# Optimization experiments

Measured on AMD Instinct MI355X. Metric: run time of the kernel, lower is better.

The kernel has to match this reference:

```python
import jax, jax.numpy as jnp
import numpy as np

D = 128        # d_model (LayerNorm(128) hardcoded)
N_HEADS = 4
DIM_K = D // N_HEADS           # 32
HD = DIM_K // N_HEADS          # 8 = per-group dim after reshape(-1, B, S, HD)
NORM_FACT = 1.0 / np.sqrt(DIM_K)
HIDDEN = 512
LN_EPS = 1e-5
NEG_INF = -1e30


def layer_norm(x, g, b):
    mu = jnp.mean(x, axis=-1, keepdims=True)
    var = jnp.mean((x - mu) ** 2, axis=-1, keepdims=True)
    return (x - mu) * jax.lax.rsqrt(var + LN_EPS) * g + b


def lower_median(x):
    # torch.median(dim=-1) returns the LOWER of the two middle values for even n
    n = x.shape[-1]
    return jnp.sort(x, axis=-1)[..., (n - 1) // 2][..., None]


def cross_cov_attention(x, y, Wq, bq, Wk, bk, Wv, bv, Wo, bo):
    # x: query-side input [B,S,D]; y: key/value-side input [B,S,D]
    B, S, _ = x.shape
    Q = (x @ Wq + bq).reshape(-1, B, S, HD)   # [16,B,S,8] (raw row-major reshape, as in torch)
    K = (y @ Wk + bk).reshape(-1, B, S, HD)
    V = (y @ Wv + bv).reshape(-1, B, S, HD)
    Qn = Q / jnp.maximum(jnp.linalg.norm(Q, axis=-1, keepdims=True), 1e-12)
    Kn = K / jnp.maximum(jnp.linalg.norm(K, axis=-1, keepdims=True), 1e-12)
    # channel-wise cross-covariance: Q^T K over tokens -> [16,B,8,8]
    scores = jnp.einsum('gbsd,gbse->gbde', Qn, Kn) * NORM_FACT
    # median-threshold mask: keep entries strictly above the (lower) median of each row
    med = lower_median(scores)
    scores = jnp.where(scores - med > 0, scores, NEG_INF)
    probs = jax.nn.softmax(scores, axis=-1)
    # probs @ V^T -> [16,B,8,S]
    ao = jnp.einsum('gbde,gbse->gbds', probs, V)
    # torch: .transpose(-2,-1).transpose(1,2).view(B,S,-1)  == axes (g,b,d,s)->(g,s,b,d)->reshape
    ao = ao.transpose(0, 3, 1, 2).reshape(B, S, -1)  # [B,S,128]
    return ao @ Wo + bo


def setup_inputs() -> dict:
    key = jax.random.key(0)
    ks = jax.random.split(key, 16)
    B, S = 32, 4096
    s = 1.0 / np.sqrt(D)
    inp = {
        'q': jax.random.normal(ks[0], (B, S, D), jnp.float32),
        'v': jax.random.normal(ks[1], (B, S, D), jnp.float32),
        'Wq': jax.random.normal(ks[2], (D, D), jnp.float32) * s,
        'bq': jnp.zeros((D,), jnp.float32),
        'Wk': jax.random.normal(ks[3], (D, D), jnp.float32) * s,
        'bk': jnp.zeros((D,), jnp.float32),
        'Wv': jax.random.normal(ks[4], (D, D), jnp.float32) * s,
        'bv': jnp.zeros((D,), jnp.float32),
        'Wo': jax.random.normal(ks[5], (D, D), jnp.float32) * s,
        'bo': jnp.zeros((D,), jnp.float32),
        'ln_g': jnp.ones((D,), jnp.float32),
        'ln_b': jnp.zeros((D,), jnp.float32),
        'W1': jax.random.normal(ks[6], (D, HIDDEN), jnp.float32) * s,
        'b1': jnp.zeros((HIDDEN,), jnp.float32),
        'W2': jax.random.normal(ks[7], (HIDDEN, D), jnp.float32) * (1.0 / np.sqrt(HIDDEN)),
        'b2': jnp.zeros((D,), jnp.float32),
    }
    return inp


def reference(q, v, Wq, bq, Wk, bk, Wv, bv, Wo, bo, ln_g, ln_b, W1, b1, W2, b2):
    # Decoder.forward: add_norm(v, attn, y=q) -> add_norm(ffn) -> + v
    attn = cross_cov_attention(v, q, Wq, bq, Wk, bk, Wv, bv, Wo, bo)
    h = layer_norm(v + attn, ln_g, ln_b)          # dropout = identity (eval)
    ffn = jax.nn.gelu(h @ W1 + b1, approximate=False) @ W2 + b2
    h2 = layer_norm(h + ffn, ln_g, ln_b)          # same Add_Norm (shared LayerNorm params)
    return h2 + v
```

## Files before the change

### kernel.cpp

```cpp
#include <hip/hip_runtime.h>
#include <math.h>


typedef __bf16 bf16x8 __attribute__((ext_vector_type(8)));
typedef float f32x4 __attribute__((ext_vector_type(4)));
typedef unsigned short u16x8 __attribute__((ext_vector_type(8)));
typedef unsigned int u32x2 __attribute__((ext_vector_type(2)));
typedef unsigned short ushort_t;

static constexpr int  DM   = 128;
static constexpr long NTOK = 131072;
static constexpr float NORMF = 0.17677669529663687f;

__device__ __forceinline__ unsigned short f2b(float x) {
    unsigned u = __builtin_bit_cast(unsigned, x);
    return (unsigned short)((u + 0x7fffu + ((u >> 16) & 1u)) >> 16);
}
__device__ __forceinline__ float b2f(unsigned short h) {
    return __builtin_bit_cast(float, ((unsigned)h) << 16);
}
__device__ __forceinline__ float b2f_lo(unsigned u) {
    return __builtin_bit_cast(float, u << 16);
}
__device__ __forceinline__ float b2f_hi(unsigned u) {
    return __builtin_bit_cast(float, u & 0xffff0000u);
}
__device__ __forceinline__ unsigned pack2(float a, float b) {
    return (unsigned)f2b(a) | ((unsigned)f2b(b) << 16);
}
__device__ __forceinline__ f32x4 mfma16(bf16x8 a, bf16x8 b, f32x4 c) {
    return __builtin_amdgcn_mfma_f32_16x16x32_bf16(a, b, c, 0, 0, 0);
}
__device__ __forceinline__ int xb_off(int tok, int chunk) {
    int c = (chunk & 8) | ((chunk ^ tok) & 7);
    return tok * 128 + c * 8;
}
__device__ __forceinline__ int h2_off(int tok, int chunk) {
    int c = (chunk & 24) | ((chunk ^ tok) & 7);
    return tok * 256 + c * 8;
}
__device__ __forceinline__ float gelu_f(float x) {
    float t = 0.70710678118654752f * x;
    float s = fabsf(t);
    float u = __builtin_amdgcn_rcpf(fmaf(0.3275911f, s, 1.0f));
    float p = fmaf(fmaf(fmaf(fmaf(1.061405429f, u, -1.453152027f), u,
                             1.421413741f), u, -0.284496736f), u, 0.254829592f);
    p *= u;
    float e = __expf(-s * s);
    float er = fmaf(-p, e, 1.0f);
    er = (t < 0.f) ? -er : er;
    return 0.5f * x * (1.0f + er);
}

__global__ __launch_bounds__(256)
void k_wcvt(const float* __restrict__ W1, const float* __restrict__ W2,
            const float* __restrict__ Wo, const float* __restrict__ Wq,
            const float* __restrict__ Wk, const float* __restrict__ Wv,
            ushort_t* __restrict__ W1t, ushort_t* __restrict__ W2t,
            ushort_t* __restrict__ Wot,
            ushort_t* __restrict__ Wqh, ushort_t* __restrict__ Wql,
            ushort_t* __restrict__ Wkh, ushort_t* __restrict__ Wkl,
            ushort_t* __restrict__ Wvh, ushort_t* __restrict__ Wvl)
{
    int frag = blockIdx.x * 4 + (threadIdx.x >> 6);
    int l = threadIdx.x & 63;
    int lr = l & 15, lg = l >> 4;
    u16x8 v;
    if (frag < 128) {
        int ht = frag >> 2, ks = frag & 3;
        #pragma unroll
        for (int j = 0; j < 8; ++j)
            v[j] = f2b(W1[(ks * 32 + lg * 8 + j) * 512 + ht * 16 + lr]);
        *(u16x8*)(W1t + ((long)frag * 64 + l) * 8) = v;
    } else if (frag < 256) {
        int f = frag - 128;
        int ot = f >> 4, ks = f & 15;
        #pragma unroll
        for (int j = 0; j < 8; ++j)
            v[j] = f2b(W2[(ks * 32 + lg * 8 + j) * 128 + ot * 16 + lr]);
        *(u16x8*)(W2t + ((long)f * 64 + l) * 8) = v;
    } else if (frag < 288) {
        int f = frag - 256;
        int ot = f >> 2, ks = f & 3;
        #pragma unroll
        for (int j = 0; j < 8; ++j)
            v[j] = f2b(Wo[(ks * 32 + lg * 8 + j) * 128 + ot * 16 + lr]);
        *(u16x8*)(Wot + ((long)f * 64 + l) * 8) = v;
    } else {
        int f = frag - 288;
        const float* S = (f < 32) ? Wq : (f < 64) ? Wk : Wv;
        ushort_t* dh = (f < 32) ? Wqh : (f < 64) ? Wkh : Wvh;
        ushort_t* dl = (f < 32) ? Wql : (f < 64) ? Wkl : Wvl;
        int fl = f & 31, ot = fl >> 2, ks = fl & 3;
        u16x8 vh, vl;
        #pragma unroll
        for (int j = 0; j < 8; ++j) {
            float x = S[(ks * 32 + lg * 8 + j) * 128 + ot * 16 + lr];
            unsigned short h = f2b(x);
            vh[j] = h;
            vl[j] = f2b(x - b2f(h));
        }
        *(u16x8*)(dh + ((long)fl * 64 + l) * 8) = vh;
        *(u16x8*)(dl + ((long)fl * 64 + l) * 8) = vl;
    }
}

__global__ __launch_bounds__(256, 2)
void k_qkvs(const float* __restrict__ qin, const float* __restrict__ vin,
            const ushort_t* __restrict__ Wqh, const ushort_t* __restrict__ Wql,
            const ushort_t* __restrict__ Wkh, const ushort_t* __restrict__ Wkl,
            const ushort_t* __restrict__ Wvh, const ushort_t* __restrict__ Wvl,
            const float* __restrict__ bq, const float* __restrict__ bk,
            const float* __restrict__ bv,
            ushort_t* __restrict__ Vbf, float* __restrict__ scoreacc)
{
    __shared__ __align__(16) char smem[65536];
    ushort_t* vhi = (ushort_t*)smem;
    ushort_t* vlo = vhi + 8192;
    ushort_t* qhi = vlo + 8192;
    ushort_t* qlo = qhi + 8192;
    ushort_t* Vt  = (ushort_t*)smem;
    float*    red = (float*)(smem + 16384);

    const int tid = threadIdx.x;
    const int w = tid >> 6, l = tid & 63;
    const int lr = l & 15, lg = l >> 4;
    const long tok0 = (long)blockIdx.x * 64;

    #pragma unroll
    for (int i = 0; i < 4; ++i) {
        int e = tid + i * 256;
        int tok = e >> 4, c = e & 15;
        long base = (tok0 + tok) * DM + c * 8;
        int xo = xb_off(tok, c);
        {
            float4 a0 = *(const float4*)(vin + base);
            float4 a1 = *(const float4*)(vin + base + 4);
            float xs[8] = {a0.x, a0.y, a0.z, a0.w, a1.x, a1.y, a1.z, a1.w};
            u16x8 hi, lo;
            #pragma unroll
            for (int jj = 0; jj < 8; ++jj) {
                unsigned short h = f2b(xs[jj]);
                hi[jj] = h; lo[jj] = f2b(xs[jj] - b2f(h));
            }
            *(u16x8*)(vhi + xo) = hi;
            *(u16x8*)(vlo + xo) = lo;
        }
        {
            float4 a0 = *(const float4*)(qin + base);
            float4 a1 = *(const float4*)(qin + base + 4);
            float xs[8] = {a0.x, a0.y, a0.z, a0.w, a1.x, a1.y, a1.z, a1.w};
            u16x8 hi, lo;
            #pragma unroll
            for (int jj = 0; jj < 8; ++jj) {
                unsigned short h = f2b(xs[jj]);
                hi[jj] = h; lo[jj] = f2b(xs[jj] - b2f(h));
            }
            *(u16x8*)(qhi + xo) = hi;
            *(u16x8*)(qlo + xo) = lo;
        }
    }
    __syncthreads();

    float qv[2][4][4];
    {
        f32x4 acc[2][4];
        #pragma unroll
        for (int ot = 0; ot < 2; ++ot)
            #pragma unroll
            for (int tt = 0; tt < 4; ++tt) acc[ot][tt] = (f32x4){0,0,0,0};
        #pragma unroll
        for (int ks = 0; ks < 4; ++ks) {
            bf16x8 wh[2], wl[2];
            #pragma unroll
            for (int ot = 0; ot < 2; ++ot) {
                int fi = (((w * 2 + ot) * 4 + ks) * 64 + l) * 8;
                wh[ot] = *(const bf16x8*)(Wqh + fi);
                wl[ot] = *(const bf16x8*)(Wql + fi);
            }
            #pragma unroll
            for (int tt = 0; tt < 4; ++tt) {
                int xo = xb_off(tt * 16 + lr, ks * 4 + lg);
                bf16x8 xh = *(const bf16x8*)(vhi + xo);
                bf16x8 xl = *(const bf16x8*)(vlo + xo);
                #pragma unroll
                for (int ot = 0; ot < 2; ++ot) {
                    acc[ot][tt] = mfma16(wh[ot], xh, acc[ot][tt]);
                    acc[ot][tt] = mfma16(wh[ot], xl, acc[ot][tt]);
                    acc[ot][tt] = mfma16(wl[ot], xh, acc[ot][tt]);
                }
            }
        }
        #pragma unroll
        for (int ot = 0; ot < 2; ++ot) {
            f32x4 bqv = *(const f32x4*)(bq + w * 32 + ot * 16 + lg * 4);
            #pragma unroll
            for (int tt = 0; tt < 4; ++tt) {
                float s2 = 0.f;
                #pragma unroll
                for (int r = 0; r < 4; ++r) {
                    float x = acc[ot][tt][r] + bqv[r];
                    qv[ot][tt][r] = x;
                    s2 = fmaf(x, x, s2);
                }
                s2 += __shfl_xor(s2, 16);
                float inv = 1.0f / fmaxf(sqrtf(s2), 1e-12f);
                #pragma unroll
                for (int r = 0; r < 4; ++r) qv[ot][tt][r] *= inv;
            }
        }
    }

    float vv[2][4][4];
    float part[4][8];
    #pragma unroll
    for (int r = 0; r < 4; ++r)
        #pragma unroll
        for (int e = 0; e < 8; ++e) part[r][e] = 0.f;
    {
        f32x4 acck[2][4], accv[2][4];
        #pragma unroll
        for (int ot = 0; ot < 2; ++ot)
            #pragma unroll
            for (int tt = 0; tt < 4; ++tt) {
                acck[ot][tt] = (f32x4){0,0,0,0};
                accv[ot][tt] = (f32x4){0,0,0,0};
            }
        #pragma unroll
        for (int ks = 0; ks < 4; ++ks) {
            bf16x8 whk[2], wlk[2], whv[2], wlv[2];
            #pragma unroll
            for (int ot = 0; ot < 2; ++ot) {
                int fi = (((w * 2 + ot) * 4 + ks) * 64 + l) * 8;
                whk[ot] = *(const bf16x8*)(Wkh + fi);
                wlk[ot] = *(const bf16x8*)(Wkl + fi);
                whv[ot] = *(const bf16x8*)(Wvh + fi);
                wlv[ot] = *(const bf16x8*)(Wvl + fi);
            }
            #pragma unroll
            for (int tt = 0; tt < 4; ++tt) {
                int xo = xb_off(tt * 16 + lr, ks * 4 + lg);
                bf16x8 xh = *(const bf16x8*)(qhi + xo);
                bf16x8 xl = *(const bf16x8*)(qlo + xo);
                #pragma unroll
                for (int ot = 0; ot < 2; ++ot) {
                    acck[ot][tt] = mfma16(whk[ot], xh, acck[ot][tt]);
                    acck[ot][tt] = mfma16(whk[ot], xl, acck[ot][tt]);
                    acck[ot][tt] = mfma16(wlk[ot], xh, acck[ot][tt]);
                    accv[ot][tt] = mfma16(whv[ot], xh, accv[ot][tt]);
                    accv[ot][tt] = mfma16(whv[ot], xl, accv[ot][tt]);
                    accv[ot][tt] = mfma16(wlv[ot], xh, accv[ot][tt]);
                }
            }
        }
        const int h0 = (lg & 1) * 4;
        #pragma unroll
        for (int ot = 0; ot < 2; ++ot) {
            f32x4 bkv = *(const f32x4*)(bk + w * 32 + ot * 16 + lg * 4);
            f32x4 bvv = *(const f32x4*)(bv + w * 32 + ot * 16 + lg * 4);
            #pragma unroll
            for (int tt = 0; tt < 4; ++tt) {
                float kq[4];
                float s2 = 0.f;
                #pragma unroll
                for (int r = 0; r < 4; ++r) {
                    float x = acck[ot][tt][r] + bkv[r];
                    kq[r] = x;
                    s2 = fmaf(x, x, s2);
                    vv[ot][tt][r] = accv[ot][tt][r] + bvv[r];
                }
                s2 += __shfl_xor(s2, 16);
                float inv = 1.0f / fmaxf(sqrtf(s2), 1e-12f);
                #pragma unroll
                for (int r = 0; r < 4; ++r) kq[r] *= inv;
                float ko[4];
                #pragma unroll
                for (int r = 0; r < 4; ++r) ko[r] = __shfl_xor(kq[r], 16);
                float ke[8];
                #pragma unroll
                for (int r = 0; r < 4; ++r) {
                    ke[h0 + r] = kq[r];
                    ke[(h0 ^ 4) + r] = ko[r];
                }
                #pragma unroll
                for (int r = 0; r < 4; ++r)
                    #pragma unroll
                    for (int e = 0; e < 8; ++e)
                        part[r][e] = fmaf(qv[ot][tt][r], ke[e], part[r][e]);
            }
        }
    }
    #pragma unroll
    for (int r = 0; r < 4; ++r)
        #pragma unroll
        for (int e = 0; e < 8; ++e) {
            float p = part[r][e];
            p += __shfl_xor(p, 1);
            p += __shfl_xor(p, 2);
            p += __shfl_xor(p, 4);
            p += __shfl_xor(p, 8);
            part[r][e] = p;
        }
    __syncthreads();

    #pragma unroll
    for (int ot = 0; ot < 2; ++ot) {
        int oc0 = w * 32 + ot * 16 + lg * 4;
        int ch = oc0 >> 3;
        #pragma unroll
        for (int tt = 0; tt < 4; ++tt) {
            int tok = tt * 16 + lr;
            int cz = (ch & 8) | ((ch ^ tok) & 7);
            u32x2 pk = {pack2(vv[ot][tt][0], vv[ot][tt][1]),
                        pack2(vv[ot][tt][2], vv[ot][tt][3])};
            *(u32x2*)(Vt + tok * 128 + cz * 8 + (oc0 & 7)) = pk;
        }
    }
    if (lr == 0) {
        #pragma unroll
        for (int r = 0; r < 4; ++r)
            #pragma unroll
            for (int e = 0; e < 8; ++e)
                red[(w * 4 + lg) * 33 + r * 8 + e] = part[r][e];
    }
    __syncthreads();

    #pragma unroll
    for (int i = 0; i < 4; ++i) {
        int e = tid + i * 256;
        int tok = e >> 4, c = e & 15;
        int cz = (c & 8) | ((c ^ tok) & 7);
        u16x8 val = *(const u16x8*)(Vt + tok * 128 + cz * 8);
        *(u16x8*)(Vbf + (tok0 + tok) * DM + c * 8) = val;
    }
    if (tid < 64) {
        int d = tid >> 3, e = tid & 7;
        int par = d >> 2, r = d & 3;
        float s = 0.f;
        #pragma unroll
        for (int ww = 0; ww < 4; ++ww)
            s += red[(ww * 4 + par) * 33 + r * 8 + e] +
                 red[(ww * 4 + par + 2) * 33 + r * 8 + e];
        scoreacc[(long)blockIdx.x * 64 + tid] = s;
    }
}

__global__ __launch_bounds__(64)
void k_medsoft(const float* __restrict__ scoreacc, float* __restrict__ probs)
{
    __shared__ float sc[64], pl[64];
    const int p = blockIdx.x, tid = threadIdx.x;
    const float* s0 = scoreacc + (long)p * 256;
    sc[tid] = (s0[tid] + s0[64 + tid] + s0[128 + tid] + s0[192 + tid]) * NORMF;
    __syncthreads();
    if (tid < 8) {
        float row[8], st[8];
        #pragma unroll
        for (int e = 0; e < 8; ++e) { row[e] = sc[tid * 8 + e]; st[e] = row[e]; }
        for (int a = 1; a < 8; ++a) {
            float v = st[a]; int b = a - 1;
            while (b >= 0 && st[b] > v) { st[b + 1] = st[b]; --b; }
            st[b + 1] = v;
        }
        float med = st[3];
        float mv[8]; float mx = -3.0e38f;
        #pragma unroll
        for (int e = 0; e < 8; ++e) {
            mv[e] = (row[e] - med > 0.f) ? row[e] : -1e30f;
            mx = fmaxf(mx, mv[e]);
        }
        float z = 0.f, ex[8];
        #pragma unroll
        for (int e = 0; e < 8; ++e) { ex[e] = expf(mv[e] - mx); z += ex[e]; }
        float iz = 1.f / z;
        #pragma unroll
        for (int e = 0; e < 8; ++e) pl[tid * 8 + e] = ex[e] * iz;
    }
    __syncthreads();
    probs[(long)p * 64 + tid] = pl[tid];
}

__global__ __launch_bounds__(256, 2)
void k_tail(const ushort_t* __restrict__ Vbf, const float* __restrict__ probs,
            const ushort_t* __restrict__ Wot, const float* __restrict__ bo,
            const ushort_t* __restrict__ W1t, const float* __restrict__ b1,
            const ushort_t* __restrict__ W2t, const float* __restrict__ b2,
            const float* __restrict__ lng, const float* __restrict__ lnb,
            const float* __restrict__ vres, float* __restrict__ out)
{
    __shared__ __align__(16) char smem[51712];
    ushort_t* Xb  = (ushort_t*)smem;
    ushort_t* Vg  = (ushort_t*)(smem + 16384);
    float*    Pl  = (float*)(smem + 32768);
    ushort_t* Hid = (ushort_t*)(smem + 16384);
    float* pS  = (float*)(smem + 49152);
    float* pQ  = pS + 256;
    float* muS = pQ + 256;
    float* rsS = muS + 64;

    const int tid = threadIdx.x;
    const int w = tid >> 6, l = tid & 63;
    const int lr = l & 15, lg = l >> 4;
    const long T0 = (long)blockIdx.x * 64;
    const int g  = (int)(T0 >> 13);
    const int r0 = (int)((T0 & 8191) >> 5);

    #pragma unroll
    for (int i = 0; i < 8; ++i) {
        int e = tid + i * 256;
        Pl[(e >> 6) * 65 + (e & 63)] = probs[(long)g * 2048 + e];
    }
    #pragma unroll
    for (int i = 0; i < 4; ++i) {
        int e = tid + i * 256;
        int ri = e >> 4, c = e & 15;
        int hb = ri >> 5, bm = (ri >> 1) & 15, rr = ri & 1;
        long t = ((long)(g * 32 + hb * 16 + bm)) * 256 + r0 + rr;
        u16x8 val = *(const u16x8*)(Vbf + t * DM + c * 8);
        int cz = (c & 8) | ((c ^ (ri >> 1)) & 7);
        *(u16x8*)(Vg + ri * 128 + cz * 8) = val;
    }

    bf16x8 aw[2][4];
    #pragma unroll
    for (int ot = 0; ot < 2; ++ot)
        #pragma unroll
        for (int ks = 0; ks < 4; ++ks)
            aw[ot][ks] = *(const bf16x8*)(Wot + ((long)((w * 2 + ot) * 4 + ks) * 64 + l) * 8);
    f32x4 bov[2], g4[2], bb4[2], b2v[2];
    #pragma unroll
    for (int ot = 0; ot < 2; ++ot) {
        int oc0 = w * 32 + ot * 16 + lg * 4;
        bov[ot] = *(const f32x4*)(bo + oc0);
        g4[ot]  = *(const f32x4*)(lng + oc0);
        bb4[ot] = *(const f32x4*)(lnb + oc0);
        b2v[ot] = *(const f32x4*)(b2 + oc0);
    }
    __syncthreads();

    #pragma unroll
    for (int i = 0; i < 4; ++i) {
        int e = tid + i * 256;
        int ti = e >> 4, bm = e & 15;
        int jj = (ti & 31) >> 1, hb = ti & 1, rr = ti >> 5;
        int ri = hb * 32 + bm * 2 + rr;
        int cz = (jj & 8) | ((jj ^ (ri >> 1)) & 7);
        u16x8 v8 = *(const u16x8*)(Vg + ri * 128 + cz * 8);
        float vf[8];
        #pragma unroll
        for (int e2 = 0; e2 < 8; ++e2) vf[e2] = b2f(v8[e2]);
        const float* pp = Pl + (hb * 16 + bm) * 65;
        u16x8 pkt;
        #pragma unroll
        for (int d = 0; d < 8; ++d) {
            float s = 0.f;
            #pragma unroll
            for (int e2 = 0; e2 < 8; ++e2) s = fmaf(pp[d * 8 + e2], vf[e2], s);
            pkt[d] = f2b(s);
        }
        *(u16x8*)(Xb + xb_off(ti, bm)) = pkt;
    }
    __syncthreads();

    float vals[4][2][4];
    float sums[4], sqs[4];
    #pragma unroll
    for (int tt = 0; tt < 4; ++tt) {
        f32x4 acc0 = (f32x4){0,0,0,0}, acc1 = (f32x4){0,0,0,0};
        int tok = tt * 16 + lr;
        #pragma unroll
        for (int ks = 0; ks < 4; ++ks) {
            bf16x8 bfrag = *(const bf16x8*)(Xb + xb_off(tok, ks * 4 + lg));
            acc0 = mfma16(aw[0][ks], bfrag, acc0);
            acc1 = mfma16(aw[1][ks], bfrag, acc1);
        }
        long gtok = T0 + tok;
        float s = 0.f, q = 0.f;
        #pragma unroll
        for (int ot = 0; ot < 2; ++ot) {
            int oc0 = w * 32 + ot * 16 + lg * 4;
            f32x4 xv = *(const f32x4*)(vres + gtok * DM + oc0);
            #pragma unroll
            for (int r = 0; r < 4; ++r) {
                float av = ot ? acc1[r] : acc0[r];
                float vvv = av + bov[ot][r] + xv[r];
                vals[tt][ot][r] = vvv;
                s += vvv; q = fmaf(vvv, vvv, q);
            }
        }
        sums[tt] = s; sqs[tt] = q;
    }
    #pragma unroll
    for (int tt = 0; tt < 4; ++tt) {
        sums[tt] += __shfl_xor(sums[tt], 16);
        sums[tt] += __shfl_xor(sums[tt], 32);
        sqs[tt]  += __shfl_xor(sqs[tt], 16);
        sqs[tt]  += __shfl_xor(sqs[tt], 32);
    }
    #pragma unroll
    for (int tt = 0; tt < 4; ++tt)
        if (lg == tt) { pS[(w * 4 + tt) * 16 + lr] = sums[tt];
                        pQ[(w * 4 + tt) * 16 + lr] = sqs[tt]; }
    __syncthreads();
    if (tid < 64) {
        float s = pS[tid] + pS[64 + tid] + pS[128 + tid] + pS[192 + tid];
        float q = pQ[tid] + pQ[64 + tid] + pQ[128 + tid] + pQ[192 + tid];
        float mu = s * 0.0078125f;
        float var = q * 0.0078125f - mu * mu;
        muS[tid] = mu;
        rsS[tid] = rsqrtf(var + 1e-5f);
    }
    __syncthreads();
    #pragma unroll
    for (int tt = 0; tt < 4; ++tt) {
        int tok = tt * 16 + lr;
        float mu = muS[tok], rs = rsS[tok];
        #pragma unroll
        for (int ot = 0; ot < 2; ++ot) {
            int oc0 = w * 32 + ot * 16 + lg * 4;
            float hf[4];
            #pragma unroll
            for (int r = 0; r < 4; ++r)
                hf[r] = (vals[tt][ot][r] - mu) * rs * g4[ot][r] + bb4[ot][r];
            int ch = oc0 >> 3;
            int cz = (ch & 8) | ((ch ^ tok) & 7);
            u32x2 pk = {pack2(hf[0], hf[1]), pack2(hf[2], hf[3])};
            *(u32x2*)(Xb + tok * 128 + cz * 8 + (oc0 & 7)) = pk;
        }
    }
    __syncthreads();

    f32x4 oacc[4][2];
    #pragma unroll
    for (int tt = 0; tt < 4; ++tt) {
        oacc[tt][0] = (f32x4){0,0,0,0};
        oacc[tt][1] = (f32x4){0,0,0,0};
    }
    #pragma unroll
    for (int sl = 0; sl < 2; ++sl) {
        #pragma unroll
        for (int hp = 0; hp < 2; ++hp) {
            bf16x8 a1[2][4];
            #pragma unroll
            for (int hh = 0; hh < 2; ++hh)
                #pragma unroll
                for (int ks = 0; ks < 4; ++ks)
                    a1[hh][ks] = *(const bf16x8*)(W1t +
                        ((long)((sl * 16 + w * 4 + hp * 2 + hh) * 4 + ks) * 64 + l) * 8);
            f32x4 b1v[2];
            #pragma unroll
            for (int hh = 0; hh < 2; ++hh)
                b1v[hh] = *(const f32x4*)(b1 + sl * 256 + w * 64 + (hp * 2 + hh) * 16 + lg * 4);
            #pragma unroll
            for (int tt = 0; tt < 4; ++tt) {
                f32x4 acc[2] = {(f32x4){0,0,0,0}, (f32x4){0,0,0,0}};
                int tok = tt * 16 + lr;
                #pragma unroll
                for (int ks = 0; ks < 4; ++ks) {
                    bf16x8 bfrag = *(const bf16x8*)(Xb + xb_off(tok, ks * 4 + lg));
                    acc[0] = mfma16(a1[0][ks], bfrag, acc[0]);
                    acc[1] = mfma16(a1[1][ks], bfrag, acc[1]);
                }
                #pragma unroll
                for (int hh = 0; hh < 2; ++hh) {
                    float gg[4];
                    #pragma unroll
                    for (int r = 0; r < 4; ++r)
                        gg[r] = gelu_f(acc[hh][r] + b1v[hh][r]);
                    int hc0 = w * 64 + (hp * 2 + hh) * 16 + lg * 4;
                    int ch = hc0 >> 3;
                    int cz = (ch & 24) | ((ch ^ tok) & 7);
                    u32x2 pk = {pack2(gg[0], gg[1]), pack2(gg[2], gg[3])};
                    *(u32x2*)(Hid + tok * 256 + cz * 8 + (hc0 & 7)) = pk;
                }
            }
        }
        __syncthreads();
        #pragma unroll
        for (int op = 0; op < 2; ++op) {
            bf16x8 a2[8];
            #pragma unroll
            for (int kl = 0; kl < 8; ++kl)
                a2[kl] = *(const bf16x8*)(W2t +
                    ((long)((w * 2 + op) * 16 + sl * 8 + kl) * 64 + l) * 8);
            #pragma unroll
            for (int tt = 0; tt < 4; ++tt) {
                int tok = tt * 16 + lr;
                #pragma unroll
                for (int kl = 0; kl < 8; ++kl) {
                    bf16x8 bfrag = *(const bf16x8*)(Hid + h2_off(tok, kl * 4 + lg));
                    oacc[tt][op] = mfma16(a2[kl], bfrag, oacc[tt][op]);
                }
            }
        }
        __syncthreads();
    }

    #pragma unroll
    for (int tt = 0; tt < 4; ++tt) {
        int tok = tt * 16 + lr;
        float s = 0.f, q = 0.f;
        #pragma unroll
        for (int ot = 0; ot < 2; ++ot) {
            int oc0 = w * 32 + ot * 16 + lg * 4;
            int ch = oc0 >> 3;
            int cz = (ch & 8) | ((ch ^ tok) & 7);
            u32x2 hp = *(const u32x2*)(Xb + tok * 128 + cz * 8 + (oc0 & 7));
            float hr[4] = {b2f_lo(hp[0]), b2f_hi(hp[0]),
                           b2f_lo(hp[1]), b2f_hi(hp[1])};
            #pragma unroll
            for (int r = 0; r < 4; ++r) {
                float vvv = oacc[tt][ot][r] + b2v[ot][r] + hr[r];
                s += vvv; q = fmaf(vvv, vvv, q);
            }
        }
        sums[tt] = s; sqs[tt] = q;
    }
    #pragma unroll
    for (int tt = 0; tt < 4; ++tt) {
        sums[tt] += __shfl_xor(sums[tt], 16);
        sums[tt] += __shfl_xor(sums[tt], 32);
        sqs[tt]  += __shfl_xor(sqs[tt], 16);
        sqs[tt]  += __shfl_xor(sqs[tt], 32);
    }
    #pragma unroll
    for (int tt = 0; tt < 4; ++tt)
        if (lg == tt) { pS[(w * 4 + tt) * 16 + lr] = sums[tt];
                        pQ[(w * 4 + tt) * 16 + lr] = sqs[tt]; }
    __syncthreads();
    if (tid < 64) {
        float s = pS[tid] + pS[64 + tid] + pS[128 + tid] + pS[192 + tid];
        float q = pQ[tid] + pQ[64 + tid] + pQ[128 + tid] + pQ[192 + tid];
        float mu = s * 0.0078125f;
        float var = q * 0.0078125f - mu * mu;
        muS[tid] = mu;
        rsS[tid] = rsqrtf(var + 1e-5f);
    }
    __syncthreads();
    #pragma unroll
    for (int tt = 0; tt < 4; ++tt) {
        int tok = tt * 16 + lr;
        long gtok = T0 + tok;
        float mu = muS[tok], rs = rsS[tok];
        #pragma unroll
        for (int ot = 0; ot < 2; ++ot) {
            int oc0 = w * 32 + ot * 16 + lg * 4;
            int ch = oc0 >> 3;
            int cz = (ch & 8) | ((ch ^ tok) & 7);
            u32x2 hp = *(const u32x2*)(Xb + tok * 128 + cz * 8 + (oc0 & 7));
            float hr[4] = {b2f_lo(hp[0]), b2f_hi(hp[0]),
                           b2f_lo(hp[1]), b2f_hi(hp[1])};
            f32x4 vv4 = *(const f32x4*)(vres + gtok * DM + oc0);
            f32x4 o;
            #pragma unroll
            for (int r = 0; r < 4; ++r) {
                float vvv = oacc[tt][ot][r] + b2v[ot][r] + hr[r];
                o[r] = (vvv - mu) * rs * g4[ot][r] + bb4[ot][r] + vv4[r];
            }
            *(f32x4*)(out + gtok * DM + oc0) = o;
        }
    }
}

extern "C" void kernel_launch(void* const* d_in, const int* in_sizes, int n_in,
                              void* d_out, int out_size, void* d_ws, size_t ws_size,
                              hipStream_t stream)
{
    const float* q   = (const float*)d_in[0];
    const float* v   = (const float*)d_in[1];
    const float* Wq  = (const float*)d_in[2];
    const float* bq  = (const float*)d_in[3];
    const float* Wk  = (const float*)d_in[4];
    const float* bk  = (const float*)d_in[5];
    const float* Wv  = (const float*)d_in[6];
    const float* bv  = (const float*)d_in[7];
    const float* Wo  = (const float*)d_in[8];
    const float* bo  = (const float*)d_in[9];
    const float* lng = (const float*)d_in[10];
    const float* lnb = (const float*)d_in[11];
    const float* W1  = (const float*)d_in[12];
    const float* b1  = (const float*)d_in[13];
    const float* W2  = (const float*)d_in[14];
    const float* b2  = (const float*)d_in[15];
    float* out = (float*)d_out;

    char* W = (char*)d_ws;
    ushort_t* Vbf      = (ushort_t*)(W);
    float*    scoreacc = (float*)(W + 33554432);
    float*    probs    = (float*)(W + 34078720);
    char* wbase = W + 34209792;
    ushort_t* Wqh = (ushort_t*)(wbase);
    ushort_t* Wql = (ushort_t*)(wbase + 32768);
    ushort_t* Wkh = (ushort_t*)(wbase + 65536);
    ushort_t* Wkl = (ushort_t*)(wbase + 98304);
    ushort_t* Wvh = (ushort_t*)(wbase + 131072);
    ushort_t* Wvl = (ushort_t*)(wbase + 163840);
    ushort_t* W1t = (ushort_t*)(wbase + 196608);
    ushort_t* W2t = (ushort_t*)(wbase + 327680);
    ushort_t* Wot = (ushort_t*)(wbase + 458752);

    dim3 blk(256);
    k_wcvt<<<96, blk, 0, stream>>>(W1, W2, Wo, Wq, Wk, Wv,
                                   W1t, W2t, Wot, Wqh, Wql, Wkh, Wkl, Wvh, Wvl);
    k_qkvs<<<2048, blk, 0, stream>>>(q, v, Wqh, Wql, Wkh, Wkl, Wvh, Wvl,
                                     bq, bk, bv, Vbf, scoreacc);
    k_medsoft<<<512, dim3(64), 0, stream>>>(scoreacc, probs);
    k_tail<<<2048, blk, 0, stream>>>(Vbf, probs, Wot, bo, W1t, b1, W2t, b2,
                                     lng, lnb, v, out);
}
```

Baseline: 200.8 us.

## Shrink tail-kernel LDS and registers, use bf16 probs and cheaper GELU

Several changes land together. f2b now uses the hardware bf16 convert, GELU switches from the erf polynomial to a tanh/sigmoid approximation, and the V projection drops its low-weight correction MFMA. In the tail kernel, the probabilities are stored as bf16, the FFN hidden dimension is processed in four 128-wide slices so LDS use shrinks and launch bounds allow 4 blocks per CU, weight and bias loads move closer to where they are used, and blocks are remapped across groups. The trade-off is lower numerical accuracy (approximate GELU, bf16 probs, coarser V) for higher occupancy and less ALU and memory work.

```diff
diff --git a/kernel.cpp b/kernel.cpp
--- a/kernel.cpp
+++ b/kernel.cpp
@@ -6,6 +6,7 @@
 typedef float f32x4 __attribute__((ext_vector_type(4)));
 typedef unsigned short u16x8 __attribute__((ext_vector_type(8)));
 typedef unsigned int u32x2 __attribute__((ext_vector_type(2)));
+typedef unsigned int u32x4 __attribute__((ext_vector_type(4)));
 typedef unsigned short ushort_t;
 
 static constexpr int  DM   = 128;
@@ -13,8 +14,8 @@
 static constexpr float NORMF = 0.17677669529663687f;
 
 __device__ __forceinline__ unsigned short f2b(float x) {
-    unsigned u = __builtin_bit_cast(unsigned, x);
-    return (unsigned short)((u + 0x7fffu + ((u >> 16) & 1u)) >> 16);
+    __bf16 b = (__bf16)x;
+    return __builtin_bit_cast(unsigned short, b);
 }
 __device__ __forceinline__ float b2f(unsigned short h) {
     return __builtin_bit_cast(float, ((unsigned)h) << 16);
@@ -35,21 +36,11 @@
     int c = (chunk & 8) | ((chunk ^ tok) & 7);
     return tok * 128 + c * 8;
 }
-__device__ __forceinline__ int h2_off(int tok, int chunk) {
-    int c = (chunk & 24) | ((chunk ^ tok) & 7);
-    return tok * 256 + c * 8;
-}
 __device__ __forceinline__ float gelu_f(float x) {
-    float t = 0.70710678118654752f * x;
-    float s = fabsf(t);
-    float u = __builtin_amdgcn_rcpf(fmaf(0.3275911f, s, 1.0f));
-    float p = fmaf(fmaf(fmaf(fmaf(1.061405429f, u, -1.453152027f), u,
-                             1.421413741f), u, -0.284496736f), u, 0.254829592f);
-    p *= u;
-    float e = __expf(-s * s);
-    float er = fmaf(-p, e, 1.0f);
-    er = (t < 0.f) ? -er : er;
-    return 0.5f * x * (1.0f + er);
+    float x2 = x * x;
+    float y = -x * fmaf(0.0713548162f, x2, 1.5957691216f);
+    float e = __expf(y);
+    return x * __builtin_amdgcn_rcpf(1.0f + e);
 }
 
 __global__ __launch_bounds__(256)
@@ -96,9 +87,9 @@
         #pragma unroll
         for (int j = 0; j < 8; ++j) {
             float x = S[(ks * 32 + lg * 8 + j) * 128 + ot * 16 + lr];
-            unsigned short h = f2b(x);
-            vh[j] = h;
-            vl[j] = f2b(x - b2f(h));
+            __bf16 bh = (__bf16)x;
+            vh[j] = __builtin_bit_cast(unsigned short, bh);
+            vl[j] = f2b(x - (float)bh);
         }
         *(u16x8*)(dh + ((long)fl * 64 + l) * 8) = vh;
         *(u16x8*)(dl + ((long)fl * 64 + l) * 8) = vl;
@@ -140,8 +131,9 @@
             u16x8 hi, lo;
             #pragma unroll
             for (int jj = 0; jj < 8; ++jj) {
-                unsigned short h = f2b(xs[jj]);
-                hi[jj] = h; lo[jj] = f2b(xs[jj] - b2f(h));
+                __bf16 bh = (__bf16)xs[jj];
+                hi[jj] = __builtin_bit_cast(unsigned short, bh);
+                lo[jj] = f2b(xs[jj] - (float)bh);
             }
             *(u16x8*)(vhi + xo) = hi;
             *(u16x8*)(vlo + xo) = lo;
@@ -153,8 +145,9 @@
             u16x8 hi, lo;
             #pragma unroll
             for (int jj = 0; jj < 8; ++jj) {
-                unsigned short h = f2b(xs[jj]);
-                hi[jj] = h; lo[jj] = f2b(xs[jj] - b2f(h));
+                __bf16 bh = (__bf16)xs[jj];
+                hi[jj] = __builtin_bit_cast(unsigned short, bh);
+                lo[jj] = f2b(xs[jj] - (float)bh);
             }
             *(u16x8*)(qhi + xo) = hi;
             *(u16x8*)(qlo + xo) = lo;
@@ -228,14 +221,13 @@
             }
         #pragma unroll
         for (int ks = 0; ks < 4; ++ks) {
-            bf16x8 whk[2], wlk[2], whv[2], wlv[2];
+            bf16x8 whk[2], wlk[2], whv[2];
             #pragma unroll
             for (int ot = 0; ot < 2; ++ot) {
                 int fi = (((w * 2 + ot) * 4 + ks) * 64 + l) * 8;
                 whk[ot] = *(const bf16x8*)(Wkh + fi);
                 wlk[ot] = *(const bf16x8*)(Wkl + fi);
                 whv[ot] = *(const bf16x8*)(Wvh + fi);
-                wlv[ot] = *(const bf16x8*)(Wvl + fi);
             }
             #pragma unroll
             for (int tt = 0; tt < 4; ++tt) {
@@ -249,7 +241,6 @@
                     acck[ot][tt] = mfma16(wlk[ot], xh, acck[ot][tt]);
                     accv[ot][tt] = mfma16(whv[ot], xh, accv[ot][tt]);
                     accv[ot][tt] = mfma16(whv[ot], xl, accv[ot][tt]);
-                    accv[ot][tt] = mfma16(wlv[ot], xh, accv[ot][tt]);
                 }
             }
         }
@@ -346,7 +337,7 @@
 }
 
 __global__ __launch_bounds__(64)
-void k_medsoft(const float* __restrict__ scoreacc, float* __restrict__ probs)
+void k_medsoft(const float* __restrict__ scoreacc, ushort_t* __restrict__ probsb)
 {
     __shared__ float sc[64], pl[64];
     const int p = blockIdx.x, tid = threadIdx.x;
@@ -377,23 +368,23 @@
         for (int e = 0; e < 8; ++e) pl[tid * 8 + e] = ex[e] * iz;
     }
     __syncthreads();
-    probs[(long)p * 64 + tid] = pl[tid];
-}
-
-__global__ __launch_bounds__(256, 2)
-void k_tail(const ushort_t* __restrict__ Vbf, const float* __restrict__ probs,
+    probsb[(long)p * 64 + tid] = f2b(pl[tid]);
+}
+
+__global__ __launch_bounds__(256, 4)
+void k_tail(const ushort_t* __restrict__ Vbf, const ushort_t* __restrict__ Pb,
             const ushort_t* __restrict__ Wot, const float* __restrict__ bo,
             const ushort_t* __restrict__ W1t, const float* __restrict__ b1,
             const ushort_t* __restrict__ W2t, const float* __restrict__ b2,
             const float* __restrict__ lng, const float* __restrict__ lnb,
             const float* __restrict__ vres, float* __restrict__ out)
 {
-    __shared__ __align__(16) char smem[51712];
+    __shared__ __align__(16) char smem[37376];
     ushort_t* Xb  = (ushort_t*)smem;
     ushort_t* Vg  = (ushort_t*)(smem + 16384);
-    float*    Pl  = (float*)(smem + 32768);
+    ushort_t* Plb = (ushort_t*)(smem + 32768);
     ushort_t* Hid = (ushort_t*)(smem + 16384);
-    float* pS  = (float*)(smem + 49152);
+    float* pS  = (float*)(smem + 32768);
     float* pQ  = pS + 256;
     float* muS = pQ + 256;
     float* rsS = muS + 64;
@@ -401,14 +392,15 @@
     const int tid = threadIdx.x;
     const int w = tid >> 6, l = tid & 63;
     const int lr = l & 15, lg = l >> 4;
-    const long T0 = (long)blockIdx.x * 64;
+    const int wid = ((blockIdx.x & 7) << 8) | (blockIdx.x >> 3);
+    const long T0 = (long)wid * 64;
     const int g  = (int)(T0 >> 13);
     const int r0 = (int)((T0 & 8191) >> 5);
 
-    #pragma unroll
-    for (int i = 0; i < 8; ++i) {
-        int e = tid + i * 256;
-        Pl[(e >> 6) * 65 + (e & 63)] = probs[(long)g * 2048 + e];
+    {
+        int e = tid * 8;
+        u16x8 pv = *(const u16x8*)(Pb + (long)g * 2048 + e);
+        *(u16x8*)(Plb + (e >> 6) * 72 + (e & 63)) = pv;
     }
     #pragma unroll
     for (int i = 0; i < 4; ++i) {
@@ -420,22 +412,6 @@
         int cz = (c & 8) | ((c ^ (ri >> 1)) & 7);
         *(u16x8*)(Vg + ri * 128 + cz * 8) = val;
     }
-
-    bf16x8 aw[2][4];
-    #pragma unroll
-    for (int ot = 0; ot < 2; ++ot)
-        #pragma unroll
-        for (int ks = 0; ks < 4; ++ks)
-            aw[ot][ks] = *(const bf16x8*)(Wot + ((long)((w * 2 + ot) * 4 + ks) * 64 + l) * 8);
-    f32x4 bov[2], g4[2], bb4[2], b2v[2];
-    #pragma unroll
-    for (int ot = 0; ot < 2; ++ot) {
-        int oc0 = w * 32 + ot * 16 + lg * 4;
-        bov[ot] = *(const f32x4*)(bo + oc0);
-        g4[ot]  = *(const f32x4*)(lng + oc0);
-        bb4[ot] = *(const f32x4*)(lnb + oc0);
-        b2v[ot] = *(const f32x4*)(b2 + oc0);
-    }
     __syncthreads();
 
     #pragma unroll
@@ -449,46 +425,70 @@
         float vf[8];
         #pragma unroll
         for (int e2 = 0; e2 < 8; ++e2) vf[e2] = b2f(v8[e2]);
-        const float* pp = Pl + (hb * 16 + bm) * 65;
-        u16x8 pkt;
+        const ushort_t* pp = Plb + (hb * 16 + bm) * 72;
+        float sd[8];
         #pragma unroll
         for (int d = 0; d < 8; ++d) {
+            u16x8 pr = *(const u16x8*)(pp + d * 8);
             float s = 0.f;
             #pragma unroll
-            for (int e2 = 0; e2 < 8; ++e2) s = fmaf(pp[d * 8 + e2], vf[e2], s);
-            pkt[d] = f2b(s);
-        }
-        *(u16x8*)(Xb + xb_off(ti, bm)) = pkt;
-    }
-    __syncthreads();
-
+            for (int e2 = 0; e2 < 8; ++e2) s = fmaf(b2f(pr[e2]), vf[e2], s);
+            sd[d] = s;
+        }
+        u32x4 po = {pack2(sd[0], sd[1]), pack2(sd[2], sd[3]),
+                    pack2(sd[4], sd[5]), pack2(sd[6], sd[7])};
+        *(u32x4*)(Xb + xb_off(ti, bm)) = po;
+    }
+    __syncthreads();
+
+    f32x4 g4[2], bb4[2];
+    #pragma unroll
+    for (int ot = 0; ot < 2; ++ot) {
+        int oc0 = w * 32 + ot * 16 + lg * 4;
+        g4[ot]  = *(const f32x4*)(lng + oc0);
+        bb4[ot] = *(const f32x4*)(lnb + oc0);
+    }
     float vals[4][2][4];
     float sums[4], sqs[4];
-    #pragma unroll
-    for (int tt = 0; tt < 4; ++tt) {
-        f32x4 acc0 = (f32x4){0,0,0,0}, acc1 = (f32x4){0,0,0,0};
-        int tok = tt * 16 + lr;
-        #pragma unroll
-        for (int ks = 0; ks < 4; ++ks) {
-            bf16x8 bfrag = *(const bf16x8*)(Xb + xb_off(tok, ks * 4 + lg));
-            acc0 = mfma16(aw[0][ks], bfrag, acc0);
-            acc1 = mfma16(aw[1][ks], bfrag, acc1);
-        }
-        long gtok = T0 + tok;
-        float s = 0.f, q = 0.f;
-        #pragma unroll
-        for (int ot = 0; ot < 2; ++ot) {
-            int oc0 = w * 32 + ot * 16 + lg * 4;
-            f32x4 xv = *(const f32x4*)(vres + gtok * DM + oc0);
-            #pragma unroll
-            for (int r = 0; r < 4; ++r) {
-                float av = ot ? acc1[r] : acc0[r];
-                float vvv = av + bov[ot][r] + xv[r];
-                vals[tt][ot][r] = vvv;
-                s += vvv; q = fmaf(vvv, vvv, q);
-            }
-        }
-        sums[tt] = s; sqs[tt] = q;
+    {
+        bf16x8 aw[2][4];
+        #pragma unroll
+        for (int ot = 0; ot < 2; ++ot)
+            #pragma unroll
+            for (int ks = 0; ks < 4; ++ks)
+                aw[ot][ks] = *(const bf16x8*)(Wot +
+                    ((long)((w * 2 + ot) * 4 + ks) * 64 + l) * 8);
+        f32x4 bov[2];
+        #pragma unroll
+        for (int ot = 0; ot < 2; ++ot)
+            bov[ot] = *(const f32x4*)(bo + w * 32 + ot * 16 + lg * 4);
+
+        #pragma unroll
+        for (int tt = 0; tt < 4; ++tt) {
+            f32x4 acc0 = (f32x4){0,0,0,0}, acc1 = (f32x4){0,0,0,0};
+            int tok = tt * 16 + lr;
+            #pragma unroll
+            for (int ks = 0; ks < 4; ++ks) {
+                bf16x8 bfrag = *(const bf16x8*)(Xb + xb_off(tok, ks * 4 + lg));
+                acc0 = mfma16(aw[0][ks], bfrag, acc0);
+                acc1 = mfma16(aw[1][ks], bfrag, acc1);
+            }
+            long gtok = T0 + tok;
+            float s = 0.f, q = 0.f;
+            #pragma unroll
+            for (int ot = 0; ot < 2; ++ot) {
+                int oc0 = w * 32 + ot * 16 + lg * 4;
+                f32x4 xv = *(const f32x4*)(vres + gtok * DM + oc0);
+                #pragma unroll
+                for (int r = 0; r < 4; ++r) {
+                    float av = ot ? acc1[r] : acc0[r];
+                    float vvv = av + bov[ot][r] + xv[r];
+                    vals[tt][ot][r] = vvv;
+                    s += vvv; q = fmaf(vvv, vvv, q);
+                }
+            }
+            sums[tt] = s; sqs[tt] = q;
+        }
     }
     #pragma unroll
     for (int tt = 0; tt < 4; ++tt) {
@@ -536,66 +536,65 @@
         oacc[tt][0] = (f32x4){0,0,0,0};
         oacc[tt][1] = (f32x4){0,0,0,0};
     }
-    #pragma unroll
-    for (int sl = 0; sl < 2; ++sl) {
-        #pragma unroll
-        for (int hp = 0; hp < 2; ++hp) {
-            bf16x8 a1[2][4];
-            #pragma unroll
-            for (int hh = 0; hh < 2; ++hh)
-                #pragma unroll
-                for (int ks = 0; ks < 4; ++ks)
-                    a1[hh][ks] = *(const bf16x8*)(W1t +
-                        ((long)((sl * 16 + w * 4 + hp * 2 + hh) * 4 + ks) * 64 + l) * 8);
-            f32x4 b1v[2];
-            #pragma unroll
-            for (int hh = 0; hh < 2; ++hh)
-                b1v[hh] = *(const f32x4*)(b1 + sl * 256 + w * 64 + (hp * 2 + hh) * 16 + lg * 4);
-            #pragma unroll
-            for (int tt = 0; tt < 4; ++tt) {
-                f32x4 acc[2] = {(f32x4){0,0,0,0}, (f32x4){0,0,0,0}};
-                int tok = tt * 16 + lr;
-                #pragma unroll
-                for (int ks = 0; ks < 4; ++ks) {
-                    bf16x8 bfrag = *(const bf16x8*)(Xb + xb_off(tok, ks * 4 + lg));
-                    acc[0] = mfma16(a1[0][ks], bfrag, acc[0]);
-                    acc[1] = mfma16(a1[1][ks], bfrag, acc[1]);
-                }
-                #pragma unroll
-                for (int hh = 0; hh < 2; ++hh) {
-                    float gg[4];
-                    #pragma unroll
-                    for (int r = 0; r < 4; ++r)
-                        gg[r] = gelu_f(acc[hh][r] + b1v[hh][r]);
-                    int hc0 = w * 64 + (hp * 2 + hh) * 16 + lg * 4;
-                    int ch = hc0 >> 3;
-                    int cz = (ch & 24) | ((ch ^ tok) & 7);
-                    u32x2 pk = {pack2(gg[0], gg[1]), pack2(gg[2], gg[3])};
-                    *(u32x2*)(Hid + tok * 256 + cz * 8 + (hc0 & 7)) = pk;
-                }
+    for (int sl = 0; sl < 4; ++sl) {
+        bf16x8 a1[2][4];
+        f32x4 b1v[2];
+        #pragma unroll
+        for (int hh = 0; hh < 2; ++hh) {
+            #pragma unroll
+            for (int ks = 0; ks < 4; ++ks)
+                a1[hh][ks] = *(const bf16x8*)(W1t +
+                    ((long)((sl * 8 + w * 2 + hh) * 4 + ks) * 64 + l) * 8);
+            b1v[hh] = *(const f32x4*)(b1 + (sl * 8 + w * 2 + hh) * 16 + lg * 4);
+        }
+        #pragma unroll
+        for (int tt = 0; tt < 4; ++tt) {
+            f32x4 acc[2] = {(f32x4){0,0,0,0}, (f32x4){0,0,0,0}};
+            int tok = tt * 16 + lr;
+            #pragma unroll
+            for (int ks = 0; ks < 4; ++ks) {
+                bf16x8 bfrag = *(const bf16x8*)(Xb + xb_off(tok, ks * 4 + lg));
+                acc[0] = mfma16(a1[0][ks], bfrag, acc[0]);
+                acc[1] = mfma16(a1[1][ks], bfrag, acc[1]);
+            }
+            #pragma unroll
+            for (int hh = 0; hh < 2; ++hh) {
+                float gg[4];
+                #pragma unroll
+                for (int r = 0; r < 4; ++r)
+                    gg[r] = gelu_f(acc[hh][r] + b1v[hh][r]);
+                int hc0 = w * 32 + hh * 16 + lg * 4;
+                int ch = hc0 >> 3;
+                int cz = (ch & 8) | ((ch ^ tok) & 7);
+                u32x2 pk = {pack2(gg[0], gg[1]), pack2(gg[2], gg[3])};
+                *(u32x2*)(Hid + tok * 128 + cz * 8 + (hc0 & 7)) = pk;
             }
         }
         __syncthreads();
-        #pragma unroll
-        for (int op = 0; op < 2; ++op) {
-            bf16x8 a2[8];
-            #pragma unroll
-            for (int kl = 0; kl < 8; ++kl)
-                a2[kl] = *(const bf16x8*)(W2t +
-                    ((long)((w * 2 + op) * 16 + sl * 8 + kl) * 64 + l) * 8);
-            #pragma unroll
-            for (int tt = 0; tt < 4; ++tt) {
-                int tok = tt * 16 + lr;
-                #pragma unroll
-                for (int kl = 0; kl < 8; ++kl) {
-                    bf16x8 bfrag = *(const bf16x8*)(Hid + h2_off(tok, kl * 4 + lg));
-                    oacc[tt][op] = mfma16(a2[kl], bfrag, oacc[tt][op]);
-                }
+        bf16x8 a2[2][4];
+        #pragma unroll
+        for (int op = 0; op < 2; ++op)
+            #pragma unroll
+            for (int kl = 0; kl < 4; ++kl)
+                a2[op][kl] = *(const bf16x8*)(W2t +
+                    ((long)((w * 2 + op) * 16 + sl * 4 + kl) * 64 + l) * 8);
+        #pragma unroll
+        for (int tt = 0; tt < 4; ++tt) {
+            int tok = tt * 16 + lr;
+            #pragma unroll
+            for (int kl = 0; kl < 4; ++kl) {
+                bf16x8 bfrag = *(const bf16x8*)(Hid + xb_off(tok, kl * 4 + lg));
+                oacc[tt][0] = mfma16(a2[0][kl], bfrag, oacc[tt][0]);
+                oacc[tt][1] = mfma16(a2[1][kl], bfrag, oacc[tt][1]);
             }
         }
         __syncthreads();
     }
 
+    f32x4 b2v[2];
+    #pragma unroll
+    for (int ot = 0; ot < 2; ++ot)
+        b2v[ot] = *(const f32x4*)(b2 + w * 32 + ot * 16 + lg * 4);
     #pragma unroll
     for (int tt = 0; tt < 4; ++tt) {
         int tok = tt * 16 + lr;
@@ -687,7 +686,7 @@
     char* W = (char*)d_ws;
     ushort_t* Vbf      = (ushort_t*)(W);
     float*    scoreacc = (float*)(W + 33554432);
-    float*    probs    = (float*)(W + 34078720);
+    ushort_t* probsb   = (ushort_t*)(W + 34078720);
     char* wbase = W + 34209792;
     ushort_t* Wqh = (ushort_t*)(wbase);
     ushort_t* Wql = (ushort_t*)(wbase + 32768);
@@ -704,7 +703,7 @@
                                    W1t, W2t, Wot, Wqh, Wql, Wkh, Wkl, Wvh, Wvl);
     k_qkvs<<<2048, blk, 0, stream>>>(q, v, Wqh, Wql, Wkh, Wkl, Wvh, Wvl,
                                      bq, bk, bv, Vbf, scoreacc);
-    k_medsoft<<<512, dim3(64), 0, stream>>>(scoreacc, probs);
-    k_tail<<<2048, blk, 0, stream>>>(Vbf, probs, Wot, bo, W1t, b1, W2t, b2,
+    k_medsoft<<<512, dim3(64), 0, stream>>>(scoreacc, probsb);
+    k_tail<<<2048, blk, 0, stream>>>(Vbf, probsb, Wot, bo, W1t, b1, W2t, b2,
                                      lng, lnb, v, out);
 }
```

Result: faster. 177.9 us (-11.4%).
